# Optimization experiments

Measured on AMD Instinct MI355X. Metric: run time of the kernel, lower is better.

The kernel has to match this reference:

```python
import jax, jax.numpy as jnp
import numpy as np

E = 4      # num_ensemble
DIN = 256  # input_dim
D = 256    # d_model (output_dim)
B = 16
T = 1024
LN_EPS = 1e-5


def setup_inputs() -> dict:
    key = jax.random.key(0)
    ks = jax.random.split(key, 14)
    s = 0.02
    x = jax.random.normal(ks[0], (B, T, DIN), dtype=jnp.float32)
    in_proj_w = s * jax.random.normal(ks[1], (3, E, DIN, D), dtype=jnp.float32)
    in_proj_b = jnp.zeros((3, E, D), dtype=jnp.float32)
    mid_w = s * jax.random.normal(ks[2], (2, E, D, D), dtype=jnp.float32)
    mid_b = jnp.zeros((2, E, D), dtype=jnp.float32)
    ff_w1 = s * jax.random.normal(ks[3], (E, D, D), dtype=jnp.float32)
    ff_b1 = jnp.zeros((E, D), dtype=jnp.float32)
    ff_w2 = s * jax.random.normal(ks[4], (E, D, D), dtype=jnp.float32)
    ff_b2 = jnp.zeros((E, D), dtype=jnp.float32)
    ln_w = jnp.ones((E, D), dtype=jnp.float32)
    ln_b = jnp.zeros((E, D), dtype=jnp.float32)
    # LRU initializer (r_min=0.9, r_max=0.999)
    r_min, r_max = 0.9, 0.999
    u1 = jax.random.uniform(ks[5], (E, D), dtype=jnp.float32)
    u2 = jax.random.uniform(ks[6], (E, D), dtype=jnp.float32)
    nu_log = jnp.log(-0.5 * jnp.log(u1 * (r_max ** 2 - r_min ** 2) + r_min ** 2))
    theta_log = jnp.log(u2 * 2.0 * np.pi)
    # |lambda|^2 = exp(-2*exp(nu_log))
    gamma_log = jnp.log(jnp.sqrt(1.0 - jnp.exp(-2.0 * jnp.exp(nu_log))))
    params_log = jnp.stack([nu_log, theta_log, gamma_log], axis=0)  # (3,E,D)
    return {"x": x, "in_proj_w": in_proj_w, "in_proj_b": in_proj_b,
            "params_log": params_log, "mid_w": mid_w, "mid_b": mid_b,
            "ff_w1": ff_w1, "ff_b1": ff_b1, "ff_w2": ff_w2, "ff_b2": ff_b2,
            "ln_w": ln_w, "ln_b": ln_b}


def _forward(x, in_proj_w, in_proj_b, params_log, mid_w, mid_b,
             ff_w1, ff_b1, ff_w2, ff_b2, ln_w, ln_b):
    # in_proj: 3 ensemble linears -> u: (3, E, B, T, D)
    u = jnp.einsum('bti,keio->kebto', x, in_proj_w) + in_proj_b[:, :, None, None, :]
    input_real, input_imag, o = u[0], u[1], u[2]

    params = jnp.exp(params_log)           # (3,E,D)
    nu, theta, gamma = params[0], params[1], params[2]
    mag = jnp.exp(-nu)
    f_real = mag * jnp.cos(theta)          # (E,D)
    f_imag = mag * jnp.sin(theta)

    ir = gamma[:, None, None, :] * input_real  # (E,B,T,D)
    ii = gamma[:, None, None, :] * input_imag

    # complex linear recurrence h_t = f * h_{t-1} + u_t over time axis
    fr = f_real[:, None, :]                # (E,1,D) broadcast over B
    fi = f_imag[:, None, :]
    ir_t = jnp.moveaxis(ir, 2, 0)          # (T,E,B,D)
    ii_t = jnp.moveaxis(ii, 2, 0)

    def step(carry, ut):
        hr, hi = carry
        ur, ui = ut
        hr2 = fr * hr - fi * hi + ur
        hi2 = fr * hi + fi * hr + ui
        return (hr2, hi2), (hr2, hi2)

    h0 = (jnp.zeros((E, B, D), x.dtype), jnp.zeros((E, B, D), x.dtype))
    (hr_last, hi_last), (out_r_t, out_i_t) = jax.lax.scan(step, h0, (ir_t, ii_t))
    output_real = jnp.moveaxis(out_r_t, 0, 2)  # (E,B,T,D)
    output_imag = jnp.moveaxis(out_i_t, 0, 2)

    # hidden packing: (1, B, 2*E*D) with ensemble blocks concatenated, real then imag
    hr_pack = jnp.transpose(hr_last, (1, 0, 2)).reshape(B, E * D)
    hi_pack = jnp.transpose(hi_last, (1, 0, 2)).reshape(B, E * D)
    hidden = jnp.concatenate([hr_pack, hi_pack], axis=-1)[None]  # (1,B,2ED)

    # middle_proj: 2 ensemble linears applied to (real, imag)
    stacked = jnp.stack([output_real, output_imag], axis=0)  # (2,E,B,T,D)
    mid = jnp.einsum('kebtd,kedo->kebto', stacked, mid_w) + mid_b[:, :, None, None, :]
    out = mid[0] - mid[1] + o                                # (E,B,T,D)

    # EnsemblePositionWiseFeedForward (dropout=0 -> identity)
    h1 = jax.nn.gelu(jnp.einsum('ebtd,edo->ebto', out, ff_w1)
                     + ff_b1[:, None, None, :], approximate=False)
    h2 = jnp.einsum('ebtd,edo->ebto', h1, ff_w2) + ff_b2[:, None, None, :] + out
    # LayerNorm over joint (E, D) dims for each (b, t)
    mean = jnp.mean(h2, axis=(0, 3), keepdims=True)
    var = jnp.var(h2, axis=(0, 3), keepdims=True)
    out_ln = (h2 - mean) / jnp.sqrt(var + LN_EPS)
    out_ln = out_ln * ln_w[:, None, None, :] + ln_b[:, None, None, :]
    return out_ln, hidden


def reference(x, in_proj_w, in_proj_b, params_log, mid_w, mid_b,
              ff_w1, ff_b1, ff_w2, ff_b2, ln_w, ln_b):
    return _forward(x, in_proj_w, in_proj_b, params_log, mid_w, mid_b,
                    ff_w1, ff_b1, ff_w2, ff_b2, ln_w, ln_b)
```

## Files before the change

### kernel.cpp

```cpp
#include <hip/hip_runtime.h>
#include <stdint.h>

#define BT_ 16384
#define TT  1024
#define CHUNKS 32
#define CLEN   32
#define LANES  16384

typedef __bf16 bf16x8 __attribute__((ext_vector_type(8)));
typedef float  f32x4  __attribute__((ext_vector_type(4)));
typedef unsigned int u32x4 __attribute__((ext_vector_type(4)));
typedef unsigned short u16;

__device__ __forceinline__ float b2f(u16 s){
    union { float f; unsigned int u; } c; c.u = ((unsigned int)s) << 16; return c.f;
}
__device__ __forceinline__ u16 f2b(float f){
    union { float f; unsigned int u; } c; c.f = f;
    unsigned int u = c.u;
    return (u16)((u + 0x7fffu + ((u >> 16) & 1u)) >> 16);
}

__device__ __forceinline__ void gload_lds16(const u16* g, u16* lds){
    __builtin_amdgcn_global_load_lds(
        (const __attribute__((address_space(1))) void*)g,
        (__attribute__((address_space(3))) void*)lds, 16, 0, 0);
}

__global__ __launch_bounds__(256) void conv_k(const float* __restrict__ x, u16* __restrict__ xc)
{
    long i = ((long)blockIdx.x * 256 + threadIdx.x) * 8;
    float4 v0 = *reinterpret_cast<const float4*>(x + i);
    float4 v1 = *reinterpret_cast<const float4*>(x + i + 4);
    union { u16 s[8]; u32x4 v; } p;
    p.s[0] = f2b(v0.x); p.s[1] = f2b(v0.y); p.s[2] = f2b(v0.z); p.s[3] = f2b(v0.w);
    p.s[4] = f2b(v1.x); p.s[5] = f2b(v1.y); p.s[6] = f2b(v1.z); p.s[7] = f2b(v1.w);
    *reinterpret_cast<u32x4*>(xc + i) = p.v;
}

__global__ __launch_bounds__(256) void prep_w(
    const float* __restrict__ ipw, const float* __restrict__ mw,
    const float* __restrict__ fw1, const float* __restrict__ fw2,
    u16* __restrict__ d_ipw, u16* __restrict__ d_mw,
    u16* __restrict__ d_fw1, u16* __restrict__ d_fw2)
{
    __shared__ u16 tile[64][72];
    int blk = blockIdx.x;
    int w = blk >> 4, t = blk & 15;
    int tr = (t >> 2) * 64;
    int tc = (t & 3) * 64;
    const float* src; u16* dst; int ostride; float sign = 1.f;
    if (w < 12)      { src = ipw + (size_t)w * 65536; dst = d_ipw + (size_t)w * 65536; ostride = 256; }
    else if (w < 20) { int u = w - 12, c = u >> 2, e = u & 3;
                       src = mw + (size_t)u * 65536;
                       dst = d_mw + (size_t)e * 131072 + c * 256; ostride = 512;
                       if (c) sign = -1.f; }
    else if (w < 24) { int e = w - 20; src = fw1 + (size_t)e * 65536; dst = d_fw1 + (size_t)e * 65536; ostride = 256; }
    else             { int e = w - 24; src = fw2 + (size_t)e * 65536; dst = d_fw2 + (size_t)e * 65536; ostride = 256; }

    int q = threadIdx.x;
    int r = q >> 2, cb = (q & 3) * 16;
#pragma unroll
    for (int j = 0; j < 4; j++) {
        int col = cb + j * 4;
        const float4 v = *reinterpret_cast<const float4*>(src + (size_t)(tr + r) * 256 + tc + col);
        tile[r][col + 0] = f2b(v.x * sign);
        tile[r][col + 1] = f2b(v.y * sign);
        tile[r][col + 2] = f2b(v.z * sign);
        tile[r][col + 3] = f2b(v.w * sign);
    }
    __syncthreads();
    int ol = q >> 2, ib = (q & 3) * 16;
    union { u16 s[8]; u32x4 v; } p0, p1;
#pragma unroll
    for (int k = 0; k < 8; k++) { p0.s[k] = tile[ib + k][ol]; p1.s[k] = tile[ib + 8 + k][ol]; }
    u16* drow = dst + (size_t)(tc + ol) * ostride + tr + ib;
    *reinterpret_cast<u32x4*>(drow)     = p0.v;
    *reinterpret_cast<u32x4*>(drow + 8) = p1.v;
}

__global__ __launch_bounds__(256, 5) void gemm_k(
    const u16* __restrict__ A0, const u16* __restrict__ B0,
    const float* __restrict__ biasf, const u16* __restrict__ aux,
    const float* __restrict__ gamlogf, u16* __restrict__ out0,
    u16* __restrict__ out1, int K, int mode)
{
    __shared__ __align__(16) u16 Bs[64 * 256];

    int tid  = threadIdx.x;
    int wave = tid >> 6, lane = tid & 63;
    int quad = lane >> 4, l16 = lane & 15;
    int m0 = blockIdx.x * 128, n0 = blockIdx.y * 64;
    int z = blockIdx.z;
    int e, k3 = 0;
    const u16* A;
    const u16* Bm;
    if (mode == 1) { k3 = z >> 2; e = z & 3; A = A0; }
    else           { e = z; A = A0 + (size_t)e * BT_ * K; }
    Bm = B0 + (size_t)(mode == 1 ? z : e) * 256 * K;

    f32x4 acc[2][4];
#pragma unroll
    for (int i = 0; i < 2; i++)
#pragma unroll
        for (int j = 0; j < 4; j++) acc[i][j] = (f32x4){0.f, 0.f, 0.f, 0.f};

    int srow = lane >> 5, schunk = lane & 31;
    int nhalf = K >> 8;

    for (int kh = 0; kh < nhalf; kh++) {
        if (kh) __syncthreads();
#pragma unroll
        for (int i = 0; i < 8; i++) {
            int row = wave * 16 + i * 2 + srow;
            int c = schunk ^ (row & 7);
            gload_lds16(Bm + (size_t)(n0 + row) * K + kh * 256 + c * 8,
                        &Bs[(wave * 16 + i * 2) * 256]);
        }
        __syncthreads();

        const u16* Arow0 = A + (size_t)(m0 + wave * 32 + l16) * K + kh * 256 + quad * 8;
        const u16* Arow1 = Arow0 + (size_t)16 * K;

        bf16x8 a0[8], a1[8];
#pragma unroll
        for (int p = 0; p < 2; p++) {
            union { u32x4 v; bf16x8 b; } u0, u1;
            u0.v = *reinterpret_cast<const u32x4*>(Arow0 + p * 32); a0[p] = u0.b;
            u1.v = *reinterpret_cast<const u32x4*>(Arow1 + p * 32); a1[p] = u1.b;
        }
#pragma unroll
        for (int kt = 0; kt < 8; kt++) {
            if (kt < 6) {
                union { u32x4 v; bf16x8 b; } u0, u1;
                u0.v = *reinterpret_cast<const u32x4*>(Arow0 + (kt + 2) * 32); a0[kt + 2] = u0.b;
                u1.v = *reinterpret_cast<const u32x4*>(Arow1 + (kt + 2) * 32); a1[kt + 2] = u1.b;
            }
#pragma unroll
            for (int nf = 0; nf < 4; nf++) {
                int row = nf * 16 + l16;
                int c = (kt * 4 + quad) ^ (row & 7);
                union { u32x4 v; bf16x8 b; } u;
                u.v = *reinterpret_cast<const u32x4*>(&Bs[row * 256 + c * 8]);
                acc[0][nf] = __builtin_amdgcn_mfma_f32_16x16x32_bf16(a0[kt], u.b, acc[0][nf], 0, 0, 0);
                acc[1][nf] = __builtin_amdgcn_mfma_f32_16x16x32_bf16(a1[kt], u.b, acc[1][nf], 0, 0, 0);
            }
        }
    }

    float bias_nf[4], gam_nf[4];
#pragma unroll
    for (int nf = 0; nf < 4; nf++) {
        int col = n0 + nf * 16 + l16;
        if (mode == 1) {
            bias_nf[nf] = biasf[z * 256 + col];
            gam_nf[nf] = (k3 < 2) ? expf(gamlogf[2048 + e * 256 + col]) : 1.f;
        } else if (mode == 2) {
            bias_nf[nf] = biasf[e * 256 + col] - biasf[1024 + e * 256 + col];
        } else {
            bias_nf[nf] = biasf[e * 256 + col];
        }
    }

    __syncthreads();
    float* fs = reinterpret_cast<float*>(Bs) + wave * 2048;
#pragma unroll
    for (int mf = 0; mf < 2; mf++)
#pragma unroll
        for (int nf = 0; nf < 4; nf++)
#pragma unroll
            for (int r = 0; r < 4; r++) {
                float v = acc[mf][nf][r] + bias_nf[nf];
                if (mode == 1) v *= gam_nf[nf];
                if (mode == 3) v = 0.5f * v * (1.0f + erff(v * 0.70710678118654752f));
                fs[(mf * 16 + quad * 4 + r) * 64 + nf * 16 + l16] = v;
            }

    int rr = lane >> 3, ch = lane & 7;
#pragma unroll
    for (int i = 0; i < 4; i++) {
        int rl = i * 8 + rr;
        int grow = m0 + wave * 32 + rl;
        const f32x4* sp = reinterpret_cast<const f32x4*>(fs + rl * 64 + ch * 8);
        f32x4 v0 = sp[0], v1 = sp[1];
        float w[8] = { v0[0], v0[1], v0[2], v0[3], v1[0], v1[1], v1[2], v1[3] };
        u16* dstp;
        if (mode == 1) {
            if (k3 < 2) dstp = out0 + (((size_t)(e * BT_ + grow)) * 2 + k3) * 256 + n0 + ch * 8;
            else        dstp = out1 + ((size_t)e * BT_ + grow) * 256 + n0 + ch * 8;
        } else {
            dstp = out0 + ((size_t)e * BT_ + grow) * 256 + n0 + ch * 8;
        }
        if (mode == 2 || mode == 4) {
            const u16* ap = aux + ((size_t)e * BT_ + grow) * 256 + n0 + ch * 8;
            u32x4 av = *reinterpret_cast<const u32x4*>(ap);
#pragma unroll
            for (int j = 0; j < 4; j++) {
                w[2 * j]     += b2f((u16)(av[j] & 0xffffu));
                w[2 * j + 1] += b2f((u16)(av[j] >> 16));
            }
        }
        union { u16 s[8]; u32x4 v; } p;
#pragma unroll
        for (int j = 0; j < 8; j++) p.s[j] = f2b(w[j]);
        *reinterpret_cast<u32x4*>(dstp) = p.v;
    }
}

__global__ __launch_bounds__(256) void scan_a(const u16* __restrict__ u,
    const float* __restrict__ plog, float2* __restrict__ carry)
{
    int l2 = blockIdx.x * 256 + threadIdx.x;
    int chunk = blockIdx.y;
    int dd = (l2 & 127) * 2, b = (l2 >> 7) & 15, e = l2 >> 11;
    float nu0 = expf(plog[e * 256 + dd]),        nu1 = expf(plog[e * 256 + dd + 1]);
    float th0 = expf(plog[1024 + e * 256 + dd]), th1 = expf(plog[1024 + e * 256 + dd + 1]);
    float m0 = expf(-nu0), m1 = expf(-nu1);
    float fr0 = m0 * cosf(th0), fi0 = m0 * sinf(th0);
    float fr1 = m1 * cosf(th1), fi1 = m1 * sinf(th1);
    size_t base = ((size_t)e * BT_ + b * TT) * 512 + (size_t)chunk * CLEN * 512 + dd;
    float hr0 = 0.f, hi0 = 0.f, hr1 = 0.f, hi1 = 0.f;
    for (int t = 0; t < CLEN; t++) {
        unsigned int wr = *reinterpret_cast<const unsigned int*>(u + base);
        unsigned int wi = *reinterpret_cast<const unsigned int*>(u + base + 256);
        float ur0 = b2f((u16)wr), ur1 = b2f((u16)(wr >> 16));
        float ui0 = b2f((u16)wi), ui1 = b2f((u16)(wi >> 16));
        float a0 = fr0 * hr0 - fi0 * hi0 + ur0;
        float b0 = fr0 * hi0 + fi0 * hr0 + ui0;
        float a1 = fr1 * hr1 - fi1 * hi1 + ur1;
        float b1 = fr1 * hi1 + fi1 * hr1 + ui1;
        hr0 = a0; hi0 = b0; hr1 = a1; hi1 = b1;
        base += 512;
    }
    size_t ci = (size_t)chunk * LANES + (size_t)e * 4096 + b * 256 + dd;
    *reinterpret_cast<float4*>(&carry[ci]) = make_float4(hr0, hi0, hr1, hi1);
}

__global__ __launch_bounds__(256) void scan_b(const float* __restrict__ plog,
                                              float2* __restrict__ carry)
{
    int l = blockIdx.x * 256 + threadIdx.x;
    int d = l & 255, e = l >> 12;
    float nu = expf(plog[e * 256 + d]);
    float th = expf(plog[1024 + e * 256 + d]);
    float magL = expf(-nu * (float)CLEN);
    float ang = th * (float)CLEN;
    float frL = magL * cosf(ang), fiL = magL * sinf(ang);
    float gr = 0.f, gi = 0.f;
    for (int j = 0; j < CHUNKS; j++) {
        float2 c = carry[(size_t)j * LANES + l];
        carry[(size_t)j * LANES + l] = make_float2(gr, gi);
        float gr2 = frL * gr - fiL * gi + c.x;
        float gi2 = frL * gi + fiL * gr + c.y;
        gr = gr2; gi = gi2;
    }
}

__global__ __launch_bounds__(256) void scan_c(u16* __restrict__ u,
    const float* __restrict__ plog, const float2* __restrict__ carry,
    float* __restrict__ outh)
{
    int l2 = blockIdx.x * 256 + threadIdx.x;
    int chunk = blockIdx.y;
    int dd = (l2 & 127) * 2, b = (l2 >> 7) & 15, e = l2 >> 11;
    float nu0 = expf(plog[e * 256 + dd]),        nu1 = expf(plog[e * 256 + dd + 1]);
    float th0 = expf(plog[1024 + e * 256 + dd]), th1 = expf(plog[1024 + e * 256 + dd + 1]);
    float m0 = expf(-nu0), m1 = expf(-nu1);
    float fr0 = m0 * cosf(th0), fi0 = m0 * sinf(th0);
    float fr1 = m1 * cosf(th1), fi1 = m1 * sinf(th1);
    size_t base = ((size_t)e * BT_ + b * TT) * 512 + (size_t)chunk * CLEN * 512 + dd;
    size_t ci = (size_t)chunk * LANES + (size_t)e * 4096 + b * 256 + dd;
    float4 c0 = *reinterpret_cast<const float4*>(&carry[ci]);
    float hr0 = c0.x, hi0 = c0.y, hr1 = c0.z, hi1 = c0.w;
    for (int t = 0; t < CLEN; t++) {
        unsigned int wr = *reinterpret_cast<const unsigned int*>(u + base);
        unsigned int wi = *reinterpret_cast<const unsigned int*>(u + base + 256);
        float ur0 = b2f((u16)wr), ur1 = b2f((u16)(wr >> 16));
        float ui0 = b2f((u16)wi), ui1 = b2f((u16)(wi >> 16));
        float a0 = fr0 * hr0 - fi0 * hi0 + ur0;
        float b0 = fr0 * hi0 + fi0 * hr0 + ui0;
        float a1 = fr1 * hr1 - fi1 * hi1 + ur1;
        float b1 = fr1 * hi1 + fi1 * hr1 + ui1;
        hr0 = a0; hi0 = b0; hr1 = a1; hi1 = b1;
        *reinterpret_cast<unsigned int*>(u + base) =
            (unsigned int)f2b(hr0) | ((unsigned int)f2b(hr1) << 16);
        *reinterpret_cast<unsigned int*>(u + base + 256) =
            (unsigned int)f2b(hi0) | ((unsigned int)f2b(hi1) << 16);
        base += 512;
    }
    if (chunk == CHUNKS - 1) {
        float* oh = outh + (size_t)4 * BT_ * 256;
        *reinterpret_cast<float2*>(&oh[b * 2048 + e * 256 + dd])        = make_float2(hr0, hr1);
        *reinterpret_cast<float2*>(&oh[b * 2048 + 1024 + e * 256 + dd]) = make_float2(hi0, hi1);
    }
}

__global__ __launch_bounds__(256) void ln_k(const u16* __restrict__ h2,
    const float* __restrict__ lnw, const float* __restrict__ lnb,
    float* __restrict__ out)
{
    int r = blockIdx.x;
    int d = threadIdx.x;
    float v[4]; float s1 = 0.f, s2 = 0.f;
#pragma unroll
    for (int e = 0; e < 4; e++) {
        float x = b2f(h2[((size_t)e * BT_ + r) * 256 + d]);
        v[e] = x; s1 += x; s2 += x * x;
    }
#pragma unroll
    for (int off = 32; off; off >>= 1) {
        s1 += __shfl_down(s1, off, 64);
        s2 += __shfl_down(s2, off, 64);
    }
    __shared__ float sm[8];
    int wave = threadIdx.x >> 6, lane = threadIdx.x & 63;
    if (lane == 0) { sm[wave] = s1; sm[4 + wave] = s2; }
    __syncthreads();
    float S1 = sm[0] + sm[1] + sm[2] + sm[3];
    float S2 = sm[4] + sm[5] + sm[6] + sm[7];
    float mean = S1 * (1.0f / 1024.0f);
    float var = S2 * (1.0f / 1024.0f) - mean * mean;
    float rstd = rsqrtf(var + 1e-5f);
#pragma unroll
    for (int e = 0; e < 4; e++) {
        float o = (v[e] - mean) * rstd * lnw[e * 256 + d] + lnb[e * 256 + d];
        out[((size_t)e * BT_ + r) * 256 + d] = o;
    }
}

extern "C" void kernel_launch(void* const* d_in, const int* in_sizes, int n_in,
                              void* d_out, int out_size, void* d_ws, size_t ws_size,
                              hipStream_t stream)
{
    const float* x    = (const float*)d_in[0];
    const float* ipw  = (const float*)d_in[1];
    const float* ipb  = (const float*)d_in[2];
    const float* plog = (const float*)d_in[3];
    const float* mw   = (const float*)d_in[4];
    const float* mb   = (const float*)d_in[5];
    const float* fw1  = (const float*)d_in[6];
    const float* fb1  = (const float*)d_in[7];
    const float* fw2  = (const float*)d_in[8];
    const float* fb2  = (const float*)d_in[9];
    const float* lnw  = (const float*)d_in[10];
    const float* lnb  = (const float*)d_in[11];
    float* out = (float*)d_out;

    u16* W = (u16*)d_ws;
    u16* buf_u    = W;
    u16* buf_out  = W + (size_t)33554432;
    u16* xc       = W + (size_t)33554432;
    float2* carry = (float2*)(W + (size_t)37748736);
    u16* buf_mw_t = W + (size_t)50331648;
    u16* c_ipw_t  = W + (size_t)50855936;
    u16* c_fw1_t  = W + (size_t)51642368;
    u16* c_fw2_t  = W + (size_t)51904512;
    u16* scratch  = (u16*)d_out;

    conv_k<<<2048, 256, 0, stream>>>(x, xc);
    prep_w<<<448, 256, 0, stream>>>(ipw, mw, fw1, fw2, c_ipw_t, buf_mw_t, c_fw1_t, c_fw2_t);
    gemm_k<<<dim3(128, 4, 12), 256, 0, stream>>>(xc, c_ipw_t, ipb, nullptr, plog, buf_u, scratch, 256, 1);
    scan_a<<<dim3(32, CHUNKS), 256, 0, stream>>>(buf_u, plog, carry);
    scan_b<<<64, 256, 0, stream>>>(plog, carry);
    scan_c<<<dim3(32, CHUNKS), 256, 0, stream>>>(buf_u, plog, carry, out);
    gemm_k<<<dim3(128, 4, 4), 256, 0, stream>>>(buf_u, buf_mw_t, mb, scratch, nullptr, buf_out, nullptr, 512, 2);
    gemm_k<<<dim3(128, 4, 4), 256, 0, stream>>>(buf_out, c_fw1_t, fb1, nullptr, nullptr, scratch, nullptr, 256, 3);
    gemm_k<<<dim3(128, 4, 4), 256, 0, stream>>>(scratch, c_fw2_t, fb2, buf_out, nullptr, buf_u, nullptr, 256, 4);
    ln_k<<<16384, 256, 0, stream>>>(buf_u, lnw, lnb, out);
}
```

Baseline: 343.2 us.

## Loop GEMM blocks over multiple M tiles reusing the LDS-resident weight tile

Each GEMM block now processes several 128-row M tiles in sequence. When K is 256 the B (weight) tile is loaded into LDS only once and reused across tiles, which cuts weight traffic and the number of launched blocks. The epilogue gets a separate swizzled LDS staging buffer written per 16-row half, and A prefetch depth goes from 2 to 4 k-steps. The extra LDS lowers the occupancy hint from 5 to 3 blocks, and the smaller grids reduce parallelism, especially for the K=512 GEMM, where B is still reloaded per tile.

```diff
diff --git a/kernel.cpp b/kernel.cpp
--- a/kernel.cpp
+++ b/kernel.cpp
@@ -79,18 +79,19 @@
     *reinterpret_cast<u32x4*>(drow + 8) = p1.v;
 }
 
-__global__ __launch_bounds__(256, 5) void gemm_k(
+__global__ __launch_bounds__(256, 3) void gemm_k(
     const u16* __restrict__ A0, const u16* __restrict__ B0,
     const float* __restrict__ biasf, const u16* __restrict__ aux,
     const float* __restrict__ gamlogf, u16* __restrict__ out0,
-    u16* __restrict__ out1, int K, int mode)
+    u16* __restrict__ out1, int K, int mode, int MT)
 {
     __shared__ __align__(16) u16 Bs[64 * 256];
+    __shared__ __align__(16) float fs_all[4][1024];
 
     int tid  = threadIdx.x;
     int wave = tid >> 6, lane = tid & 63;
     int quad = lane >> 4, l16 = lane & 15;
-    int m0 = blockIdx.x * 128, n0 = blockIdx.y * 64;
+    int n0 = blockIdx.y * 64;
     int z = blockIdx.z;
     int e, k3 = 0;
     const u16* A;
@@ -99,54 +100,8 @@
     else           { e = z; A = A0 + (size_t)e * BT_ * K; }
     Bm = B0 + (size_t)(mode == 1 ? z : e) * 256 * K;
 
-    f32x4 acc[2][4];
-#pragma unroll
-    for (int i = 0; i < 2; i++)
-#pragma unroll
-        for (int j = 0; j < 4; j++) acc[i][j] = (f32x4){0.f, 0.f, 0.f, 0.f};
-
     int srow = lane >> 5, schunk = lane & 31;
     int nhalf = K >> 8;
-
-    for (int kh = 0; kh < nhalf; kh++) {
-        if (kh) __syncthreads();
-#pragma unroll
-        for (int i = 0; i < 8; i++) {
-            int row = wave * 16 + i * 2 + srow;
-            int c = schunk ^ (row & 7);
-            gload_lds16(Bm + (size_t)(n0 + row) * K + kh * 256 + c * 8,
-                        &Bs[(wave * 16 + i * 2) * 256]);
-        }
-        __syncthreads();
-
-        const u16* Arow0 = A + (size_t)(m0 + wave * 32 + l16) * K + kh * 256 + quad * 8;
-        const u16* Arow1 = Arow0 + (size_t)16 * K;
-
-        bf16x8 a0[8], a1[8];
-#pragma unroll
-        for (int p = 0; p < 2; p++) {
-            union { u32x4 v; bf16x8 b; } u0, u1;
-            u0.v = *reinterpret_cast<const u32x4*>(Arow0 + p * 32); a0[p] = u0.b;
-            u1.v = *reinterpret_cast<const u32x4*>(Arow1 + p * 32); a1[p] = u1.b;
-        }
-#pragma unroll
-        for (int kt = 0; kt < 8; kt++) {
-            if (kt < 6) {
-                union { u32x4 v; bf16x8 b; } u0, u1;
-                u0.v = *reinterpret_cast<const u32x4*>(Arow0 + (kt + 2) * 32); a0[kt + 2] = u0.b;
-                u1.v = *reinterpret_cast<const u32x4*>(Arow1 + (kt + 2) * 32); a1[kt + 2] = u1.b;
-            }
-#pragma unroll
-            for (int nf = 0; nf < 4; nf++) {
-                int row = nf * 16 + l16;
-                int c = (kt * 4 + quad) ^ (row & 7);
-                union { u32x4 v; bf16x8 b; } u;
-                u.v = *reinterpret_cast<const u32x4*>(&Bs[row * 256 + c * 8]);
-                acc[0][nf] = __builtin_amdgcn_mfma_f32_16x16x32_bf16(a0[kt], u.b, acc[0][nf], 0, 0, 0);
-                acc[1][nf] = __builtin_amdgcn_mfma_f32_16x16x32_bf16(a1[kt], u.b, acc[1][nf], 0, 0, 0);
-            }
-        }
-    }
 
     float bias_nf[4], gam_nf[4];
 #pragma unroll
@@ -162,48 +117,103 @@
         }
     }
 
-    __syncthreads();
-    float* fs = reinterpret_cast<float*>(Bs) + wave * 2048;
-#pragma unroll
-    for (int mf = 0; mf < 2; mf++)
-#pragma unroll
-        for (int nf = 0; nf < 4; nf++)
-#pragma unroll
-            for (int r = 0; r < 4; r++) {
-                float v = acc[mf][nf][r] + bias_nf[nf];
-                if (mode == 1) v *= gam_nf[nf];
-                if (mode == 3) v = 0.5f * v * (1.0f + erff(v * 0.70710678118654752f));
-                fs[(mf * 16 + quad * 4 + r) * 64 + nf * 16 + l16] = v;
-            }
-
+    float* fs = fs_all[wave];
     int rr = lane >> 3, ch = lane & 7;
-#pragma unroll
-    for (int i = 0; i < 4; i++) {
-        int rl = i * 8 + rr;
-        int grow = m0 + wave * 32 + rl;
-        const f32x4* sp = reinterpret_cast<const f32x4*>(fs + rl * 64 + ch * 8);
-        f32x4 v0 = sp[0], v1 = sp[1];
-        float w[8] = { v0[0], v0[1], v0[2], v0[3], v1[0], v1[1], v1[2], v1[3] };
-        u16* dstp;
-        if (mode == 1) {
-            if (k3 < 2) dstp = out0 + (((size_t)(e * BT_ + grow)) * 2 + k3) * 256 + n0 + ch * 8;
-            else        dstp = out1 + ((size_t)e * BT_ + grow) * 256 + n0 + ch * 8;
-        } else {
-            dstp = out0 + ((size_t)e * BT_ + grow) * 256 + n0 + ch * 8;
+
+    for (int mt = 0; mt < MT; mt++) {
+        int m0 = (blockIdx.x * MT + mt) * 128;
+
+        f32x4 acc[2][4];
+#pragma unroll
+        for (int i = 0; i < 2; i++)
+#pragma unroll
+            for (int j = 0; j < 4; j++) acc[i][j] = (f32x4){0.f, 0.f, 0.f, 0.f};
+
+        for (int kh = 0; kh < nhalf; kh++) {
+            if (nhalf > 1 || mt == 0) {
+                if (mt || kh) __syncthreads();
+#pragma unroll
+                for (int i = 0; i < 8; i++) {
+                    int row = wave * 16 + i * 2 + srow;
+                    int c = schunk ^ (row & 7);
+                    gload_lds16(Bm + (size_t)(n0 + row) * K + kh * 256 + c * 8,
+                                &Bs[(wave * 16 + i * 2) * 256]);
+                }
+                __syncthreads();
+            }
+
+            const u16* Arow0 = A + (size_t)(m0 + wave * 32 + l16) * K + kh * 256 + quad * 8;
+            const u16* Arow1 = Arow0 + (size_t)16 * K;
+
+            bf16x8 a0[8], a1[8];
+#pragma unroll
+            for (int p = 0; p < 4; p++) {
+                union { u32x4 v; bf16x8 b; } u0, u1;
+                u0.v = *reinterpret_cast<const u32x4*>(Arow0 + p * 32); a0[p] = u0.b;
+                u1.v = *reinterpret_cast<const u32x4*>(Arow1 + p * 32); a1[p] = u1.b;
+            }
+#pragma unroll
+            for (int kt = 0; kt < 8; kt++) {
+                if (kt < 4) {
+                    union { u32x4 v; bf16x8 b; } u0, u1;
+                    u0.v = *reinterpret_cast<const u32x4*>(Arow0 + (kt + 4) * 32); a0[kt + 4] = u0.b;
+                    u1.v = *reinterpret_cast<const u32x4*>(Arow1 + (kt + 4) * 32); a1[kt + 4] = u1.b;
+                }
+#pragma unroll
+                for (int nf = 0; nf < 4; nf++) {
+                    int row = nf * 16 + l16;
+                    int c = (kt * 4 + quad) ^ (row & 7);
+                    union { u32x4 v; bf16x8 b; } u;
+                    u.v = *reinterpret_cast<const u32x4*>(&Bs[row * 256 + c * 8]);
+                    acc[0][nf] = __builtin_amdgcn_mfma_f32_16x16x32_bf16(a0[kt], u.b, acc[0][nf], 0, 0, 0);
+                    acc[1][nf] = __builtin_amdgcn_mfma_f32_16x16x32_bf16(a1[kt], u.b, acc[1][nf], 0, 0, 0);
+                }
+            }
         }
-        if (mode == 2 || mode == 4) {
-            const u16* ap = aux + ((size_t)e * BT_ + grow) * 256 + n0 + ch * 8;
-            u32x4 av = *reinterpret_cast<const u32x4*>(ap);
-#pragma unroll
-            for (int j = 0; j < 4; j++) {
-                w[2 * j]     += b2f((u16)(av[j] & 0xffffu));
-                w[2 * j + 1] += b2f((u16)(av[j] >> 16));
+
+#pragma unroll
+        for (int mf = 0; mf < 2; mf++) {
+#pragma unroll
+            for (int nf = 0; nf < 4; nf++) {
+                int colsw = (nf * 16 + l16) ^ (quad * 8);
+#pragma unroll
+                for (int r = 0; r < 4; r++) {
+                    float v = acc[mf][nf][r] + bias_nf[nf];
+                    if (mode == 1) v *= gam_nf[nf];
+                    if (mode == 3) v = 0.5f * v * (1.0f + erff(v * 0.70710678118654752f));
+                    fs[(quad * 4 + r) * 64 + colsw] = v;
+                }
+            }
+#pragma unroll
+            for (int i = 0; i < 2; i++) {
+                int rl = i * 8 + rr;
+                int grow = m0 + wave * 32 + mf * 16 + rl;
+                const float* sp = fs + rl * 64 + ((ch * 8) ^ ((rl >> 2) * 8));
+                f32x4 v0 = *reinterpret_cast<const f32x4*>(sp);
+                f32x4 v1 = *reinterpret_cast<const f32x4*>(sp + 4);
+                float w[8] = { v0[0], v0[1], v0[2], v0[3], v1[0], v1[1], v1[2], v1[3] };
+                u16* dstp;
+                if (mode == 1) {
+                    if (k3 < 2) dstp = out0 + (((size_t)(e * BT_ + grow)) * 2 + k3) * 256 + n0 + ch * 8;
+                    else        dstp = out1 + ((size_t)e * BT_ + grow) * 256 + n0 + ch * 8;
+                } else {
+                    dstp = out0 + ((size_t)e * BT_ + grow) * 256 + n0 + ch * 8;
+                }
+                if (mode == 2 || mode == 4) {
+                    const u16* ap = aux + ((size_t)e * BT_ + grow) * 256 + n0 + ch * 8;
+                    u32x4 av = *reinterpret_cast<const u32x4*>(ap);
+#pragma unroll
+                    for (int j = 0; j < 4; j++) {
+                        w[2 * j]     += b2f((u16)(av[j] & 0xffffu));
+                        w[2 * j + 1] += b2f((u16)(av[j] >> 16));
+                    }
+                }
+                union { u16 s[8]; u32x4 v; } p;
+#pragma unroll
+                for (int j = 0; j < 8; j++) p.s[j] = f2b(w[j]);
+                *reinterpret_cast<u32x4*>(dstp) = p.v;
             }
         }
-        union { u16 s[8]; u32x4 v; } p;
-#pragma unroll
-        for (int j = 0; j < 8; j++) p.s[j] = f2b(w[j]);
-        *reinterpret_cast<u32x4*>(dstp) = p.v;
     }
 }
 
@@ -359,12 +369,12 @@
 
     conv_k<<<2048, 256, 0, stream>>>(x, xc);
     prep_w<<<448, 256, 0, stream>>>(ipw, mw, fw1, fw2, c_ipw_t, buf_mw_t, c_fw1_t, c_fw2_t);
-    gemm_k<<<dim3(128, 4, 12), 256, 0, stream>>>(xc, c_ipw_t, ipb, nullptr, plog, buf_u, scratch, 256, 1);
+    gemm_k<<<dim3(32, 4, 12), 256, 0, stream>>>(xc, c_ipw_t, ipb, nullptr, plog, buf_u, scratch, 256, 1, 4);
     scan_a<<<dim3(32, CHUNKS), 256, 0, stream>>>(buf_u, plog, carry);
     scan_b<<<64, 256, 0, stream>>>(plog, carry);
     scan_c<<<dim3(32, CHUNKS), 256, 0, stream>>>(buf_u, plog, carry, out);
-    gemm_k<<<dim3(128, 4, 4), 256, 0, stream>>>(buf_u, buf_mw_t, mb, scratch, nullptr, buf_out, nullptr, 512, 2);
-    gemm_k<<<dim3(128, 4, 4), 256, 0, stream>>>(buf_out, c_fw1_t, fb1, nullptr, nullptr, scratch, nullptr, 256, 3);
-    gemm_k<<<dim3(128, 4, 4), 256, 0, stream>>>(scratch, c_fw2_t, fb2, buf_out, nullptr, buf_u, nullptr, 256, 4);
+    gemm_k<<<dim3(64, 4, 4), 256, 0, stream>>>(buf_u, buf_mw_t, mb, scratch, nullptr, buf_out, nullptr, 512, 2, 2);
+    gemm_k<<<dim3(64, 4, 4), 256, 0, stream>>>(buf_out, c_fw1_t, fb1, nullptr, nullptr, scratch, nullptr, 256, 3, 2);
+    gemm_k<<<dim3(64, 4, 4), 256, 0, stream>>>(scratch, c_fw2_t, fb2, buf_out, nullptr, buf_u, nullptr, 256, 4, 2);
     ln_k<<<16384, 256, 0, stream>>>(buf_u, lnw, lnb, out);
 }
```

New measurement: 329.8 us. 1.04x faster.
